# Kernel tuning notes

Measured on AMD Instinct MI355X. Metric: run time of the kernel, lower is better.

The kernel has to match this reference:

```python
import jax, jax.numpy as jnp
import numpy as np

INV_SIGMA = 10.0
EPS = 1e-8  # torch CosineSimilarity default eps


def setup_inputs() -> dict:
    key = jax.random.key(0)
    k1, k2, k3, k4 = jax.random.split(key, 4)
    n, C, G, N = 16384, 32, 128, 200000
    x = jax.random.normal(k1, (n, G), dtype=jnp.float32)
    v = jax.random.normal(k2, (n, G), dtype=jnp.float32)
    k = jax.random.randint(k3, (n, C), 0, N, dtype=jnp.int64)
    X = jax.random.normal(k4, (N, G), dtype=jnp.float32)
    return {"x": x, "v": v, "k": k, "X": X}


def reference(x, v, k, X):
    # gather neighbors: [n, C, G]
    deltas = X[k] - x[:, None, :]
    # cosine similarity along dim=2 (torch clamps norm product at eps)
    num = jnp.einsum('ng,ncg->nc', v, deltas)
    v_norm = jnp.linalg.norm(v, axis=-1)          # [n]
    d_norm = jnp.linalg.norm(deltas, axis=-1)     # [n, C]
    cs = num / jnp.maximum(v_norm[:, None] * d_norm, EPS)
    # expm1 scaling + L1-style normalization over neighbors
    Tv = jnp.expm1(cs * INV_SIGMA)
    Tv = Tv / jnp.abs(Tv).sum(axis=1, keepdims=True)
    # NaN mask on dX (same gather as deltas)
    dX = jnp.nan_to_num(deltas, nan=0.0)
    subtractor = Tv.mean(axis=1, keepdims=True) * dX.sum(axis=1)  # [n,1]*[n,G]
    v_proj = jnp.einsum('ncg,nc->ng', dX, Tv) - subtractor
    return v_proj
```

## Files before the change

kernel.cpp:

```cpp
#include <hip/hip_runtime.h>
#include <math.h>

#define GDIM 128
#define CDIM 32
#define EPSV 1e-8f
#define INV_SIGMA 10.0f
#define PAD 4

__global__ __launch_bounds__(256) void nc_kernel(
    const float* __restrict__ x, const float* __restrict__ v,
    const int*   __restrict__ k, const float* __restrict__ X,
    float* __restrict__ out)
{
    const int i = blockIdx.x;
    const int t = threadIdx.x;

    __shared__ float sdel[CDIM][GDIM + PAD];
    __shared__ float sx[GDIM];
    __shared__ float sv[GDIM];
    __shared__ int   sk[CDIM];
    __shared__ float stv[CDIM];
    __shared__ float s_vnorm;
    __shared__ float s_mean;
    __shared__ float s_acc[GDIM];
    __shared__ float s_sumd[GDIM];

    if (t < GDIM) {
        sx[t] = x[(size_t)i * GDIM + t];
        sv[t] = v[(size_t)i * GDIM + t];
    } else if (t < GDIM + CDIM) {
        sk[t - GDIM] = k[(size_t)i * CDIM + (t - GDIM)];
    }
    __syncthreads();

    {
        const int lane4 = (t & 31) * 4;
        const float4 xv = *reinterpret_cast<const float4*>(&sx[lane4]);
        #pragma unroll
        for (int r = 0; r < 4; ++r) {
            const int c = (t >> 5) + r * 8;
            const float4 Xv = *reinterpret_cast<const float4*>(
                &X[(size_t)sk[c] * GDIM + lane4]);
            float4 d;
            d.x = Xv.x - xv.x; d.y = Xv.y - xv.y;
            d.z = Xv.z - xv.z; d.w = Xv.w - xv.w;
            *reinterpret_cast<float4*>(&sdel[c][lane4]) = d;
        }
    }

    if (t < 64) {
        float a = sv[t], b = sv[t + 64];
        float vn = a * a + b * b;
        #pragma unroll
        for (int off = 32; off; off >>= 1) vn += __shfl_xor(vn, off);
        if (t == 0) s_vnorm = sqrtf(vn);
    }
    __syncthreads();

    {
        const int c = t >> 3;
        const int l = t & 7;
        float num = 0.f, ss = 0.f;
        #pragma unroll
        for (int j = 0; j < 16; ++j) {
            const int g = l + 8 * j;
            const float d = sdel[c][g];
            num = fmaf(sv[g], d, num);
            ss  = fmaf(d, d, ss);
        }
        #pragma unroll
        for (int off = 4; off; off >>= 1) {
            num += __shfl_xor(num, off);
            ss  += __shfl_xor(ss, off);
        }
        if (l == 0) {
            const float dn = sqrtf(ss);
            const float cs = num / fmaxf(s_vnorm * dn, EPSV);
            stv[c] = expm1f(cs * INV_SIGMA);
        }
    }
    __syncthreads();

    if (t < CDIM) {
        const float tv = stv[t];
        float sa = fabsf(tv), st = tv;
        #pragma unroll
        for (int off = 16; off; off >>= 1) {
            sa += __shfl_xor(sa, off);
            st += __shfl_xor(st, off);
        }
        stv[t] = tv / sa;
        if (t == 0) s_mean = (st / sa) * (1.0f / CDIM);
    }
    __syncthreads();

    {
        const int g = t & (GDIM - 1);
        const int h = t >> 7;
        float acc = 0.f, sd = 0.f;
        #pragma unroll
        for (int cc = 0; cc < 16; ++cc) {
            const int c2 = h * 16 + cc;
            const float d = sdel[c2][g];
            acc = fmaf(d, stv[c2], acc);
            sd += d;
        }
        if (h == 1) { s_acc[g] = acc; s_sumd[g] = sd; }
        __syncthreads();
        if (h == 0) {
            const float ta = acc + s_acc[g];
            const float ts = sd  + s_sumd[g];
            out[(size_t)i * GDIM + g] = ta - s_mean * ts;
        }
    }
}

extern "C" void kernel_launch(void* const* d_in, const int* in_sizes, int n_in,
                              void* d_out, int out_size, void* d_ws, size_t ws_size,
                              hipStream_t stream) {
    const float* x = (const float*)d_in[0];
    const float* v = (const float*)d_in[1];
    const int*   k = (const int*)  d_in[2];
    const float* X = (const float*)d_in[3];
    float* out = (float*)d_out;
    const int n = in_sizes[0] / GDIM;
    nc_kernel<<<n, 256, 0, stream>>>(x, v, k, X, out);
}
```

Baseline: 180.4 us.

## Issue index and gather loads up front, drop staging syncs, simplify final reduction

Removes the shared-memory staging of x, v and k and its barrier. Each thread now loads its four neighbor indices and issues all four X row gathers together with the x and v loads, so global latency overlaps before the first sync. The final projection is done by 128 threads over all 32 neighbors instead of two halves merged through shared memory and an extra barrier. A min-blocks hint of 8 is added to launch_bounds to raise occupancy, at the cost of a tighter register budget.

```diff
diff --git a/kernel.cpp b/kernel.cpp
--- a/kernel.cpp
+++ b/kernel.cpp
@@ -7,7 +7,7 @@
 #define INV_SIGMA 10.0f
 #define PAD 4
 
-__global__ __launch_bounds__(256) void nc_kernel(
+__global__ __launch_bounds__(256, 8) void nc_kernel(
     const float* __restrict__ x, const float* __restrict__ v,
     const int*   __restrict__ k, const float* __restrict__ X,
     float* __restrict__ out)
@@ -16,44 +16,47 @@
     const int t = threadIdx.x;
 
     __shared__ float sdel[CDIM][GDIM + PAD];
-    __shared__ float sx[GDIM];
     __shared__ float sv[GDIM];
-    __shared__ int   sk[CDIM];
     __shared__ float stv[CDIM];
     __shared__ float s_vnorm;
     __shared__ float s_mean;
-    __shared__ float s_acc[GDIM];
-    __shared__ float s_sumd[GDIM];
 
-    if (t < GDIM) {
-        sx[t] = x[(size_t)i * GDIM + t];
-        sv[t] = v[(size_t)i * GDIM + t];
-    } else if (t < GDIM + CDIM) {
-        sk[t - GDIM] = k[(size_t)i * CDIM + (t - GDIM)];
-    }
-    __syncthreads();
-
-    {
-        const int lane4 = (t & 31) * 4;
-        const float4 xv = *reinterpret_cast<const float4*>(&sx[lane4]);
-        #pragma unroll
-        for (int r = 0; r < 4; ++r) {
-            const int c = (t >> 5) + r * 8;
-            const float4 Xv = *reinterpret_cast<const float4*>(
-                &X[(size_t)sk[c] * GDIM + lane4]);
-            float4 d;
-            d.x = Xv.x - xv.x; d.y = Xv.y - xv.y;
-            d.z = Xv.z - xv.z; d.w = Xv.w - xv.w;
-            *reinterpret_cast<float4*>(&sdel[c][lane4]) = d;
-        }
+    float va = 0.f, vb = 0.f;
+    if (t < 64) {
+        va = v[(size_t)i * GDIM + t];
+        vb = v[(size_t)i * GDIM + t + 64];
     }
 
+    const int lane4 = (t & 31) * 4;
+    const int cbase = t >> 5;
+    int k0 = k[(size_t)i * CDIM + cbase];
+    int k1 = k[(size_t)i * CDIM + cbase + 8];
+    int k2 = k[(size_t)i * CDIM + cbase + 16];
+    int k3 = k[(size_t)i * CDIM + cbase + 24];
+    const float4 xv = *reinterpret_cast<const float4*>(&x[(size_t)i * GDIM + lane4]);
+    const float4 X0 = *reinterpret_cast<const float4*>(&X[(size_t)k0 * GDIM + lane4]);
+    const float4 X1 = *reinterpret_cast<const float4*>(&X[(size_t)k1 * GDIM + lane4]);
+    const float4 X2 = *reinterpret_cast<const float4*>(&X[(size_t)k2 * GDIM + lane4]);
+    const float4 X3 = *reinterpret_cast<const float4*>(&X[(size_t)k3 * GDIM + lane4]);
+
     if (t < 64) {
-        float a = sv[t], b = sv[t + 64];
-        float vn = a * a + b * b;
+        sv[t] = va; sv[t + 64] = vb;
+        float vn = va * va + vb * vb;
         #pragma unroll
         for (int off = 32; off; off >>= 1) vn += __shfl_xor(vn, off);
         if (t == 0) s_vnorm = sqrtf(vn);
+    }
+
+    {
+        float4 d;
+        d.x = X0.x - xv.x; d.y = X0.y - xv.y; d.z = X0.z - xv.z; d.w = X0.w - xv.w;
+        *reinterpret_cast<float4*>(&sdel[cbase][lane4]) = d;
+        d.x = X1.x - xv.x; d.y = X1.y - xv.y; d.z = X1.z - xv.z; d.w = X1.w - xv.w;
+        *reinterpret_cast<float4*>(&sdel[cbase + 8][lane4]) = d;
+        d.x = X2.x - xv.x; d.y = X2.y - xv.y; d.z = X2.z - xv.z; d.w = X2.w - xv.w;
+        *reinterpret_cast<float4*>(&sdel[cbase + 16][lane4]) = d;
+        d.x = X3.x - xv.x; d.y = X3.y - xv.y; d.z = X3.z - xv.z; d.w = X3.w - xv.w;
+        *reinterpret_cast<float4*>(&sdel[cbase + 24][lane4]) = d;
     }
     __syncthreads();
 
@@ -94,24 +97,16 @@
     }
     __syncthreads();
 
-    {
-        const int g = t & (GDIM - 1);
-        const int h = t >> 7;
+    if (t < GDIM) {
+        const int g = t;
         float acc = 0.f, sd = 0.f;
         #pragma unroll
-        for (int cc = 0; cc < 16; ++cc) {
-            const int c2 = h * 16 + cc;
-            const float d = sdel[c2][g];
-            acc = fmaf(d, stv[c2], acc);
+        for (int c = 0; c < CDIM; ++c) {
+            const float d = sdel[c][g];
+            acc = fmaf(d, stv[c], acc);
             sd += d;
         }
-        if (h == 1) { s_acc[g] = acc; s_sumd[g] = sd; }
-        __syncthreads();
-        if (h == 0) {
-            const float ta = acc + s_acc[g];
-            const float ts = sd  + s_sumd[g];
-            out[(size_t)i * GDIM + g] = ta - s_mean * ts;
-        }
+        out[(size_t)i * GDIM + g] = acc - s_mean * sd;
     }
 }
 
```

New measurement: 179.2 us. Within noise of the previous version (-0.7%).
